# Performance work log

Measured on AMD Instinct MI355X. Metric: run time of the kernel, lower is better.

The kernel has to match this reference:

```python
import jax, jax.numpy as jnp
import numpy as np

B = 4          # clouds per batch
N_PER = 8192   # points per cloud
RATIO = 0.5
M = int(N_PER * RATIO)   # sampled centroids per cloud
R = 0.2        # radius
K = 64         # max_num_neighbors
C_IN = 64


def setup_inputs() -> dict:
    key = jax.random.key(0)
    k1, k2, k3, k4 = jax.random.split(key, 4)
    N = B * N_PER
    x = jax.random.normal(k1, (N, C_IN), dtype=jnp.float32)
    pos = jax.random.uniform(k2, (N, 3), dtype=jnp.float32)  # unit cube
    batch = jnp.repeat(jnp.arange(B, dtype=jnp.int32), N_PER)
    W1 = jax.random.normal(k3, (C_IN + 3, 64), dtype=jnp.float32) * (1.0 / np.sqrt(C_IN + 3))
    b1 = jnp.zeros((64,), dtype=jnp.float32)
    W2 = jax.random.normal(k4, (64, 128), dtype=jnp.float32) * (1.0 / np.sqrt(64))
    b2 = jnp.zeros((128,), dtype=jnp.float32)
    return {"x": x, "pos": pos, "batch": batch, "W1": W1, "b1": b1, "W2": W2, "b2": b2}


def _fps(posb):
    """Farthest point sampling, vectorized over clouds. posb: [B, n, 3] -> idx [B, M]."""
    d0 = jnp.sum((posb - posb[:, :1]) ** 2, axis=-1)  # dist^2 to seed point 0: [B, n]

    def step(dists, _):
        far = jnp.argmax(dists, axis=1)                              # [B]
        newp = jnp.take_along_axis(posb, far[:, None, None], axis=1)  # [B, 1, 3]
        d = jnp.sum((posb - newp) ** 2, axis=-1)                      # [B, n]
        return jnp.minimum(dists, d), far.astype(jnp.int32)

    _, rest = jax.lax.scan(step, d0, None, length=M - 1)  # rest: [M-1, B]
    return jnp.concatenate([jnp.zeros((B, 1), jnp.int32), rest.T], axis=1)  # [B, M]


def reference(x, pos, batch, W1, b1, W2, b2):
    posb = pos.reshape(B, N_PER, 3)
    xb = x.reshape(B, N_PER, C_IN)

    # --- fps ---
    idx = _fps(posb)                                         # [B, M]
    q = jnp.take_along_axis(posb, idx[:, :, None], axis=1)   # sampled centroids [B, M, 3]

    # --- radius query: K nearest neighbors within radius R (same cloud) ---
    d2 = jnp.sum((q[:, :, None, :] - posb[:, None, :, :]) ** 2, axis=-1)  # [B, M, n]
    neg = jnp.where(d2 <= R * R, -d2, -jnp.inf)
    vals, nbr = jax.lax.top_k(neg, K)                        # [B, M, K]
    valid = vals > -jnp.inf                                  # neighbor mask

    # --- PointNetConv: gather -> MLP -> masked max aggregation ---
    bidx = jnp.arange(B)[:, None, None]
    xj = xb[bidx, nbr]                                       # [B, M, K, C_IN]
    rel = posb[bidx, nbr] - q[:, :, None, :]                 # [B, M, K, 3]
    feat = jnp.concatenate([xj, rel], axis=-1)               # [B, M, K, C_IN+3]
    h = jax.nn.relu(feat @ W1 + b1)                          # [B, M, K, 64]
    h = jax.nn.relu(h @ W2 + b2)                             # [B, M, K, 128]
    h = jnp.where(valid[..., None], h, -jnp.inf)
    out = jnp.max(h, axis=2)                                 # [B, M, 128]; self-edge guarantees >=1 valid

    x_out = out.reshape(B * M, 128)
    pos_out = q.reshape(B * M, 3)
    batch_out = jnp.repeat(jnp.arange(B, dtype=batch.dtype), M)
    return x_out, pos_out, batch_out
```

## Files before the change

### kernel.cpp

```cpp
#include <hip/hip_runtime.h>
#include <stdint.h>

#define NPER 8192
#define NB 4
#define MPER 4096
#define MTOT (NB*MPER)
#define KNB 64
#define CIN 64
#define R2C 0.04f

#define POSOUT_OFF (MTOT*128)
#define BATCH_OFF  (MTOT*128 + MTOT*3)

#define PRE_OFF 2162688ull
#define PRE_BYTES 8388608ull

#define SSTR 34816
#define PERM_F 29200

typedef float v2f __attribute__((ext_vector_type(2)));

#define FPS_T 1024
#define PTS 8
#define NCELL 512

#define OFF_XS 0
#define OFF_YS (OFF_XS + NPER*4)
#define OFF_ZS (OFF_YS + NPER*4)
#define OFF_OS (OFF_ZS + NPER*4)
#define OFF_WIN (OFF_OS + NPER*2)
#define OFF_HIST (OFF_WIN + MPER*2)
#define OFF_SCAN (OFF_HIST + NCELL*4)
#define OFF_SLOT (OFF_SCAN + NCELL*4)
#define OFF_SID0 (OFF_SLOT + 24)
#define OFF_BSC  (OFF_SID0 + 8)
#define FPS_LDS  (OFF_BSC + NCELL*4)

template<int CTRL>
__device__ __forceinline__ unsigned dppmax(unsigned v) {
  unsigned t = (unsigned)__builtin_amdgcn_update_dpp(
      0, (int)v, CTRL, 0xf, 0xf, true);
  return v > t ? v : t;
}
__device__ __forceinline__ unsigned wave_max_u32(unsigned v) {
  v = dppmax<0x111>(v);
  v = dppmax<0x112>(v);
  v = dppmax<0x114>(v);
  v = dppmax<0x118>(v);
  v = dppmax<0x142>(v);
  v = dppmax<0x143>(v);
  return (unsigned)__builtin_amdgcn_readlane((int)v, 63);
}

__device__ __forceinline__ unsigned brick_key(unsigned c) {
  unsigned ix = c >> 6, iy = (c >> 3) & 7, iz = c & 7;
  unsigned bid = ((ix >> 2) << 3) | ((iy >> 2) << 2) | (iz >> 1);
  unsigned lid = ((ix & 3) << 3) | ((iy & 3) << 1) | (iz & 1);
  return (bid << 5) | lid;
}

__global__ __launch_bounds__(1024) void k_fps(const float* __restrict__ pos,
                                              float* __restrict__ dout,
                                              const float* __restrict__ xin,
                                              const float* __restrict__ W1,
                                              float* __restrict__ hp)
{
#pragma clang fp contract(off)
  extern __shared__ char smem[];
  const int tid = threadIdx.x;

  if (blockIdx.x >= NB) {
    float* Ws = (float*)smem;
    float* Xs2 = (float*)(smem + 16384);
    const int row0 = (blockIdx.x - NB) * 64;
    for (int e = tid; e < 64*64; e += FPS_T) Ws[e] = W1[e];
    for (int e = tid; e < 64*64; e += FPS_T) {
      int r = e >> 6, ch = e & 63;
      Xs2[r*65 + ch] = xin[(size_t)(row0 + r) * 64 + ch];
    }
    __syncthreads();
    if (tid < 256) {
      const int rg = tid >> 4, cg = tid & 15;
      const int r0 = rg << 2, c0 = cg << 2;
      float acc[4][4];
#pragma unroll
      for (int r = 0; r < 4; ++r)
#pragma unroll
        for (int c = 0; c < 4; ++c) acc[r][c] = 0.0f;
      for (int k = 0; k < 64; ++k) {
        const float4 w = *(const float4*)&Ws[(k << 6) + c0];
        const float xr[4] = {Xs2[(r0+0)*65 + k], Xs2[(r0+1)*65 + k],
                             Xs2[(r0+2)*65 + k], Xs2[(r0+3)*65 + k]};
        const float wc[4] = {w.x, w.y, w.z, w.w};
#pragma unroll
        for (int r = 0; r < 4; ++r)
#pragma unroll
          for (int c = 0; c < 4; ++c)
            acc[r][c] = fmaf(xr[r], wc[c], acc[r][c]);
      }
#pragma unroll
      for (int r = 0; r < 4; ++r) {
        float4 o = {acc[r][0], acc[r][1], acc[r][2], acc[r][3]};
        *(float4*)&hp[(size_t)(row0 + r0 + r) * 64 + c0] = o;
      }
    }
    return;
  }

  float* Xs = (float*)(smem + OFF_XS);
  float* Ys = (float*)(smem + OFF_YS);
  float* Zs = (float*)(smem + OFF_ZS);
  unsigned short* Os = (unsigned short*)(smem + OFF_OS);
  unsigned short* winb = (unsigned short*)(smem + OFF_WIN);
  unsigned* hist = (unsigned*)(smem + OFF_HIST);
  unsigned* scanb = (unsigned*)(smem + OFF_SCAN);
  unsigned long long* slot3 = (unsigned long long*)(smem + OFF_SLOT);
  unsigned* sid0p = (unsigned*)(smem + OFF_SID0);
  unsigned* bsc = (unsigned*)(smem + OFF_BSC);

  const int b = blockIdx.x;
  const float* pb = pos + (size_t)b * NPER * 3;
  float* qo = dout + POSOUT_OFF + (size_t)b * MPER * 3;
  float* scrb = dout + (size_t)b * SSTR;
  float* gSX = scrb; float* gSY = scrb + 8192; float* gSZ = scrb + 16384;
  unsigned* gSO = (unsigned*)(scrb + 24576);
  unsigned* gCS = (unsigned*)(scrb + 28672);
  unsigned short* gPM = (unsigned short*)(scrb + PERM_F);

  if (tid < NCELL) hist[tid] = 0u;
  if (tid == 0) { slot3[0] = 0ull; slot3[1] = 0ull; slot3[2] = 0ull; }
  __syncthreads();

  float sxv[PTS], syv[PTS], szv[PTS];
  unsigned cellv[PTS];
#pragma unroll
  for (int k = 0; k < PTS; ++k) {
    int i = k * FPS_T + tid;
    sxv[k] = pb[i*3+0]; syv[k] = pb[i*3+1]; szv[k] = pb[i*3+2];
    unsigned ix = min(7u, (unsigned)(int)(sxv[k] * 8.0f));
    unsigned iy = min(7u, (unsigned)(int)(syv[k] * 8.0f));
    unsigned iz = min(7u, (unsigned)(int)(szv[k] * 8.0f));
    cellv[k] = (ix << 6) | (iy << 3) | iz;
    atomicAdd(&hist[cellv[k]], 1u);
  }
  __syncthreads();
  if (tid < NCELL) scanb[tid] = hist[tid];
  __syncthreads();
  for (int s = 1; s < NCELL; s <<= 1) {
    unsigned v = 0u;
    if (tid >= s && tid < NCELL) v = scanb[tid - s];
    __syncthreads();
    if (tid >= s && tid < NCELL) scanb[tid] += v;
    __syncthreads();
  }
  if (tid < NCELL) {
    hist[tid] = scanb[tid] - hist[tid];
    gCS[tid+1] = scanb[tid];
  }
  if (tid == 0) gCS[0] = 0u;
  __syncthreads();
  if (tid < NCELL) {
    unsigned c = (unsigned)tid;
    unsigned cntc = scanb[c] - hist[c];
    bsc[brick_key(c)] = cntc;
  }
  __syncthreads();
  for (int s = 1; s < NCELL; s <<= 1) {
    unsigned v = 0u;
    if (tid >= s && tid < NCELL) v = bsc[tid - s];
    __syncthreads();
    if (tid >= s && tid < NCELL) bsc[tid] += v;
    __syncthreads();
  }
  {
    unsigned bst = 0u;
    if (tid < NCELL) {
      unsigned c = (unsigned)tid;
      unsigned cntc = scanb[c] - hist[c];
      bst = bsc[brick_key(c)] - cntc;
    }
    __syncthreads();
    if (tid < NCELL) bsc[tid] = bst;
  }
  __syncthreads();
#pragma unroll
  for (int k = 0; k < PTS; ++k) {
    unsigned dst = atomicAdd(&hist[cellv[k]], 1u);
    unsigned p   = atomicAdd(&bsc[cellv[k]], 1u);
    int orig = k * FPS_T + tid;
    Xs[dst] = sxv[k]; Ys[dst] = syv[k]; Zs[dst] = szv[k];
    Os[dst] = (unsigned short)orig;
    gPM[p] = (unsigned short)dst;
    if (orig == 0) *sid0p = dst;
  }
  __syncthreads();
  for (int e = tid; e < NPER; e += FPS_T) {
    gSX[e] = Xs[e]; gSY[e] = Ys[e]; gSZ[e] = Zs[e];
  }
  for (int e = tid; e < NPER/2; e += FPS_T)
    gSO[e] = ((const unsigned*)Os)[e];
  v2f Xp[4], Yp[4], Zp[4], Dp[4];
  unsigned RK[PTS];
  float bxlo = 3.402823466e+38f, bylo = bxlo, bzlo = bxlo;
  float bxhi = -bxlo, byhi = bxhi, bzhi = bxhi;
#pragma unroll
  for (int k = 0; k < PTS; ++k) {
    int s = (int)gPM[tid * PTS + k];
    float xx = Xs[s], yy = Ys[s], zz = Zs[s];
    Xp[k>>1][k&1] = xx; Yp[k>>1][k&1] = yy; Zp[k>>1][k&1] = zz;
    Dp[k>>1][k&1] = 3.402823466e+38f;
    unsigned orig = Os[s];
    RK[k] = ((unsigned)(NPER - 1 - orig) << 13) | (unsigned)s;
    bxlo = fminf(bxlo, xx); bxhi = fmaxf(bxhi, xx);
    bylo = fminf(bylo, yy); byhi = fmaxf(byhi, yy);
    bzlo = fminf(bzlo, zz); bzhi = fmaxf(bzhi, zz);
  }

  unsigned long long tkey = 0ull, wkey = 0ull;
  float lmax = 3.402823466e+38f;
  unsigned sidx = *sid0p;
  for (int m = 1; m < MPER; ++m) {
    const float cx = Xs[sidx], cy = Ys[sidx], cz = Zs[sidx];
    if (tid == 0) winb[m-1] = (unsigned short)sidx;
    if (tid == 1) slot3[(m+1) % 3] = 0ull;
    float ax = fmaxf(fmaxf(__fsub_rn(bxlo, cx), __fsub_rn(cx, bxhi)), 0.0f);
    float ay = fmaxf(fmaxf(__fsub_rn(bylo, cy), __fsub_rn(cy, byhi)), 0.0f);
    float az = fmaxf(fmaxf(__fsub_rn(bzlo, cz), __fsub_rn(cz, bzhi)), 0.0f);
    float lb = ax*ax + ay*ay + az*az;
    bool upd = (lb * 0.99988f) < lmax;
    if (__ballot(upd) != 0ull) {
      if (upd) {
        v2f cx2 = {cx, cx}, cy2 = {cy, cy}, cz2 = {cz, cz};
        v2f dnp[4];
        float bd = -1.0f;
#pragma unroll
        for (int p = 0; p < 4; ++p) {
          v2f dx = Xp[p] - cx2;
          v2f dy = Yp[p] - cy2;
          v2f dz = Zp[p] - cz2;
          v2f s = (dx*dx + dy*dy) + dz*dz;
          v2f dn;
          dn.x = fminf(Dp[p].x, s.x);
          dn.y = fminf(Dp[p].y, s.y);
          Dp[p] = dn; dnp[p] = dn;
          bd = fmaxf(bd, fmaxf(dn.x, dn.y));
        }
        unsigned brk = 0u;
#pragma unroll
        for (int p = 0; p < 4; ++p) {
          brk = (dnp[p].x == bd) ? max(brk, RK[2*p])   : brk;
          brk = (dnp[p].y == bd) ? max(brk, RK[2*p+1]) : brk;
        }
        tkey = ((unsigned long long)__float_as_uint(bd) << 26) | brk;
        lmax = bd;
      }
      unsigned hi = (unsigned)(tkey >> 26);
      unsigned M = wave_max_u32(hi);
      unsigned rk = (unsigned)tkey & 0x3FFFFFFu;
      unsigned long long msk = __ballot(hi == M);
      unsigned lo;
      if (__popcll(msk) == 1) {
        int ln = (int)__builtin_ctzll(msk);
        lo = (unsigned)__builtin_amdgcn_readlane((int)rk, ln);
      } else {
        lo = wave_max_u32((hi == M) ? rk : 0u);
      }
      wkey = ((unsigned long long)M << 26) | lo;
    }
    if ((tid & 63) == 0) atomicMax(&slot3[m % 3], wkey);
    __syncthreads();
    sidx = (unsigned)(slot3[m % 3] & 0x1FFFull);
  }
  if (tid == 0) winb[MPER-1] = (unsigned short)sidx;
  __syncthreads();
  for (int e = tid; e < MPER; e += FPS_T) {
    unsigned s = winb[e];
    qo[e*3+0] = Xs[s]; qo[e*3+1] = Ys[s]; qo[e*3+2] = Zs[s];
  }
}

#define SCAP 512
__global__ __launch_bounds__(256) void k_radius(const float* __restrict__ pos,
    float* __restrict__ dout, unsigned short* __restrict__ nbr,
    int* __restrict__ cnt)
{
  __shared__ unsigned candH[4][SCAP];
  __shared__ unsigned candL[4][SCAP];
  const int wid = threadIdx.x >> 6, lane = threadIdx.x & 63;
  const int m = blockIdx.x * 4 + wid;
  const int b = m >> 12;
  const float* scrb = dout + (size_t)b * SSTR;
  const float* SX = scrb;
  const float* SY = scrb + 8192;
  const float* SZ = scrb + 16384;
  const unsigned short* SO = (const unsigned short*)(scrb + 24576);
  const unsigned* CS = (const unsigned*)(scrb + 28672);
  const float* q = dout + POSOUT_OFF + (size_t)m * 3;
  const float qx = q[0], qy = q[1], qz = q[2];
  const int ixc = min(7, (int)(qx * 8.0f));
  const int iyc = min(7, (int)(qy * 8.0f));
  const int izc = min(7, (int)(qz * 8.0f));
  const int izlo = max(izc-2, 0), izhi = min(izc+2, 7);
  unsigned s0v = 0u, s1v = 0u;
  {
    int ix = ixc + lane / 5 - 2;
    int iy = iyc + lane % 5 - 2;
    if (lane < 25 && ix >= 0 && ix < 8 && iy >= 0 && iy < 8) {
      int cb = (ix << 6) | (iy << 3);
      s0v = CS[cb + izlo];
      s1v = CS[cb + izhi + 1];
    }
  }
  unsigned cw = 0;
  for (int seg = 0; seg < 25; ++seg) {
    unsigned s0 = (unsigned)__builtin_amdgcn_readlane((int)s0v, seg);
    unsigned s1 = (unsigned)__builtin_amdgcn_readlane((int)s1v, seg);
    for (unsigned i0 = s0; i0 < s1; i0 += 64) {
      unsigned i = i0 + (unsigned)lane;
      float dx = __fsub_rn(qx, SX[i]);
      float dy = __fsub_rn(qy, SY[i]);
      float dz = __fsub_rn(qz, SZ[i]);
      float d2 = __fadd_rn(__fadd_rn(__fmul_rn(dx,dx), __fmul_rn(dy,dy)),
                           __fmul_rn(dz,dz));
      bool in = (i < s1) && (d2 <= R2C);
      unsigned long long mk = __ballot(in);
      unsigned pre = (unsigned)__popcll(mk & ((1ull << lane) - 1ull));
      if (in) {
        unsigned slot = cw + pre;
        if (slot < SCAP) {
          candH[wid][slot] = __float_as_uint(d2);
          candL[wid][slot] = (unsigned)SO[i];
        }
      }
      cw += (unsigned)__popcll(mk);
    }
  }
  if (cw > SCAP) cw = SCAP;
  for (int s = (int)cw + lane; s < SCAP; s += 64) {
    candH[wid][s] = 0xFFFFFFFFu; candL[wid][s] = 0xFFFFFFFFu;
  }
  __syncthreads();
  for (int k = 2; k <= SCAP; k <<= 1) {
    for (int j = k >> 1; j > 0; j >>= 1) {
#pragma unroll
      for (int s = 0; s < SCAP/128; ++s) {
        int t = lane + (s << 6);
        int e = ((t & ~(j-1)) << 1) | (t & (j-1));
        int p = e | j;
        unsigned aH = candH[wid][e], aL = candL[wid][e];
        unsigned cH = candH[wid][p], cL = candL[wid][p];
        bool agt = (aH > cH) || (aH == cH && aL > cL);
        bool asc = ((e & k) == 0);
        bool sw = asc ? agt : !agt && (aH != cH || aL != cL);
        if (sw) {
          candH[wid][e] = cH; candL[wid][e] = cL;
          candH[wid][p] = aH; candL[wid][p] = aL;
        }
      }
      __syncthreads();
    }
  }
  int kk = (int)cw; if (kk > KNB) kk = KNB;
  nbr[(size_t)m*KNB + lane] =
    (lane < kk) ? (unsigned short)(candL[wid][lane] & 0xFFFFu)
                : (unsigned short)0;
  if (lane == 0) {
    cnt[m] = kk;
    dout[BATCH_OFF + m] = (float)b;
  }
}

__global__ __launch_bounds__(128) void k_conv2(
    const float* __restrict__ hp, const float* __restrict__ pos,
    const float* __restrict__ W1, const float* __restrict__ b1,
    const float* __restrict__ W2, const float* __restrict__ b2,
    const unsigned short* __restrict__ nbr, const int* __restrict__ cntp,
    float* __restrict__ dout)
{
  __shared__ __align__(16) float bufA[68*68];
  __shared__ __align__(16) float bufB[16*136];
  __shared__ float w1p[3*64];
  __shared__ unsigned short nbr_s[64];
  __shared__ float qv[3];
  __shared__ int cnt_s;
  const int t = threadIdx.x;
  const int m = blockIdx.x;
  const int b = m >> 12;
  if (t < 64) nbr_s[t] = nbr[(size_t)m*KNB + t];
  else if (t == 64) cnt_s = cntp[m];
  else if (t >= 65 && t < 68) qv[t-65] = dout[POSOUT_OFF + (size_t)m*3 + (t-65)];
  for (int e = t; e < 192; e += 128) w1p[e] = W1[64*64 + e];
  __syncthreads();
  {
    const int h = t & 63, jj = t >> 6;
    const size_t hb = (size_t)b * NPER * 64;
    for (int j0 = 0; j0 < 64; j0 += 2) {
      int j = j0 + jj;
      int r = nbr_s[j];
      bufA[h*68 + j] = hp[hb + (size_t)r*64 + h];
    }
  }
  {
    const size_t pbb = (size_t)b * NPER * 3;
    for (int e = t; e < 192; e += 128) {
      int j = e & 63, d = e >> 6;
      int r = nbr_s[j];
      bufA[(64+d)*68 + j] = pos[pbb + (size_t)r*3 + d] - qv[d];
    }
  }
  __syncthreads();
  for (int e = t; e < 64*64; e += 128) {
    int h = e >> 6, j = e & 63;
    float v = bufA[h*68 + j];
    v = fmaf(bufA[64*68 + j], w1p[h],       v);
    v = fmaf(bufA[65*68 + j], w1p[64 + h],  v);
    v = fmaf(bufA[66*68 + j], w1p[128 + h], v);
    bufA[h*68 + j] = fmaxf(v + b1[h], 0.0f);
  }
  const int jg = t & 7, hg = t >> 3;
  const int j0 = jg << 3;
  const int c0 = hg << 3;
  v2f acc2p[8][4];
#pragma unroll
  for (int c = 0; c < 8; ++c)
#pragma unroll
    for (int jp = 0; jp < 4; ++jp) acc2p[c][jp] = (v2f){0.0f, 0.0f};
  for (int hc = 0; hc < 64; hc += 16) {
    __syncthreads();
    for (int e = t; e < 16*128; e += 128) {
      int hh = e >> 7, c = e & 127;
      bufB[hh*136 + c] = W2[(size_t)(hc+hh)*128 + c];
    }
    __syncthreads();
#pragma unroll
    for (int h = 0; h < 16; ++h) {
      const float4 ja = *(const float4*)&bufA[(hc+h)*68 + j0];
      const float4 jb = *(const float4*)&bufA[(hc+h)*68 + j0 + 4];
      const float4 wa = *(const float4*)&bufB[h*136 + c0];
      const float4 wb = *(const float4*)&bufB[h*136 + c0 + 4];
      const v2f hj[4] = {{ja.x, ja.y}, {ja.z, ja.w}, {jb.x, jb.y}, {jb.z, jb.w}};
      const float wv[8] = {wa.x, wa.y, wa.z, wa.w, wb.x, wb.y, wb.z, wb.w};
#pragma unroll
      for (int c = 0; c < 8; ++c) {
        const v2f w2 = {wv[c], wv[c]};
#pragma unroll
        for (int jp = 0; jp < 4; ++jp)
          acc2p[c][jp] += w2 * hj[jp];
      }
    }
  }
  const int cntv = cnt_s;
  const float4 b2a = *(const float4*)&b2[c0];
  const float4 b2b = *(const float4*)&b2[c0 + 4];
  const float bv2[8] = {b2a.x, b2a.y, b2a.z, b2a.w, b2b.x, b2b.y, b2b.z, b2b.w};
  float best[8];
#pragma unroll
  for (int c = 0; c < 8; ++c) {
    float v = -3.402823466e+38f;
#pragma unroll
    for (int jp = 0; jp < 4; ++jp) {
      float h0v = fmaxf(acc2p[c][jp].x + bv2[c], 0.0f);
      float h1v = fmaxf(acc2p[c][jp].y + bv2[c], 0.0f);
      v = (j0 + 2*jp     < cntv) ? fmaxf(v, h0v) : v;
      v = (j0 + 2*jp + 1 < cntv) ? fmaxf(v, h1v) : v;
    }
    best[c] = v;
  }
#pragma unroll
  for (int off = 1; off < 8; off <<= 1)
#pragma unroll
    for (int c = 0; c < 8; ++c)
      best[c] = fmaxf(best[c], __shfl_xor(best[c], off));
  if (jg == 0) {
    float4 o0 = {best[0], best[1], best[2], best[3]};
    float4 o1 = {best[4], best[5], best[6], best[7]};
    *(float4*)&dout[(size_t)m*128 + c0] = o0;
    *(float4*)&dout[(size_t)m*128 + c0 + 4] = o1;
  }
}

__global__ __launch_bounds__(128) void k_conv(
    const float* __restrict__ x, const float* __restrict__ pos,
    const float* __restrict__ W1, const float* __restrict__ b1,
    const float* __restrict__ W2, const float* __restrict__ b2,
    const unsigned short* __restrict__ nbr, const int* __restrict__ cntp,
    float* __restrict__ dout)
{
  __shared__ __align__(16) float bufA[68*68];
  __shared__ __align__(16) float bufB[68*68];
  __shared__ unsigned short nbr_s[64];
  __shared__ float qv[3];
  __shared__ int cnt_s;
  const int t = threadIdx.x;
  const int m = blockIdx.x;
  const int b = m >> 12;
  if (t < 64) nbr_s[t] = nbr[(size_t)m*KNB + t];
  else if (t == 64) cnt_s = cntp[m];
  else if (t >= 65 && t < 68) qv[t-65] = dout[POSOUT_OFF + (size_t)m*3 + (t-65)];
  for (int e = t; e < 67*64; e += 128) {
    int ch = e >> 6, h = e & 63;
    bufB[ch*68 + h] = W1[e];
  }
  __syncthreads();
  {
    const int ch = t & 63, jj = t >> 6;
    const size_t xb = (size_t)b * NPER * CIN;
    for (int j0 = 0; j0 < 64; j0 += 2) {
      int j = j0 + jj;
      int r = nbr_s[j];
      bufA[ch*68 + j] = x[xb + (size_t)r*CIN + ch];
    }
  }
  {
    const size_t pbb = (size_t)b * NPER * 3;
    for (int e = t; e < 192; e += 128) {
      int j = e & 63, d = e >> 6;
      int r = nbr_s[j];
      bufA[(64+d)*68 + j] = pos[pbb + (size_t)r*3 + d] - qv[d];
    }
  }
  __syncthreads();
  const int jg = t & 7, hg = t >> 3;
  const int j0 = jg << 3;
  const int h0 = hg << 2;
  v2f accp[4][4];
#pragma unroll
  for (int hh = 0; hh < 4; ++hh)
#pragma unroll
    for (int jp = 0; jp < 4; ++jp) accp[hh][jp] = (v2f){0.0f, 0.0f};
  for (int ch = 0; ch < 67; ++ch) {
    const float4 fa = *(const float4*)&bufA[ch*68 + j0];
    const float4 fb = *(const float4*)&bufA[ch*68 + j0 + 4];
    const float4 w  = *(const float4*)&bufB[ch*68 + h0];
    const v2f fj[4] = {{fa.x, fa.y}, {fa.z, fa.w}, {fb.x, fb.y}, {fb.z, fb.w}};
    const float ws4[4] = {w.x, w.y, w.z, w.w};
#pragma unroll
    for (int hh = 0; hh < 4; ++hh) {
      const v2f wv2 = {ws4[hh], ws4[hh]};
#pragma unroll
      for (int jp = 0; jp < 4; ++jp)
        accp[hh][jp] += wv2 * fj[jp];
    }
  }
  __syncthreads();
  {
    const float4 bb = *(const float4*)&b1[h0];
    const float bv[4] = {bb.x, bb.y, bb.z, bb.w};
#pragma unroll
    for (int hh = 0; hh < 4; ++hh) {
      float4 o0, o1;
      o0.x = fmaxf(accp[hh][0].x + bv[hh], 0.0f);
      o0.y = fmaxf(accp[hh][0].y + bv[hh], 0.0f);
      o0.z = fmaxf(accp[hh][1].x + bv[hh], 0.0f);
      o0.w = fmaxf(accp[hh][1].y + bv[hh], 0.0f);
      o1.x = fmaxf(accp[hh][2].x + bv[hh], 0.0f);
      o1.y = fmaxf(accp[hh][2].y + bv[hh], 0.0f);
      o1.z = fmaxf(accp[hh][3].x + bv[hh], 0.0f);
      o1.w = fmaxf(accp[hh][3].y + bv[hh], 0.0f);
      *(float4*)&bufA[(h0+hh)*68 + j0] = o0;
      *(float4*)&bufA[(h0+hh)*68 + j0 + 4] = o1;
    }
  }
  const int c0 = hg << 3;
  v2f acc2p[8][4];
#pragma unroll
  for (int c = 0; c < 8; ++c)
#pragma unroll
    for (int jp = 0; jp < 4; ++jp) acc2p[c][jp] = (v2f){0.0f, 0.0f};
  for (int hc = 0; hc < 64; hc += 16) {
    __syncthreads();
    for (int e = t; e < 16*128; e += 128) {
      int hh = e >> 7, c = e & 127;
      bufB[hh*136 + c] = W2[(size_t)(hc+hh)*128 + c];
    }
    __syncthreads();
#pragma unroll
    for (int h = 0; h < 16; ++h) {
      const float4 ja = *(const float4*)&bufA[(hc+h)*68 + j0];
      const float4 jb = *(const float4*)&bufA[(hc+h)*68 + j0 + 4];
      const float4 wa = *(const float4*)&bufB[h*136 + c0];
      const float4 wb = *(const float4*)&bufB[h*136 + c0 + 4];
      const v2f hj[4] = {{ja.x, ja.y}, {ja.z, ja.w}, {jb.x, jb.y}, {jb.z, jb.w}};
      const float wv[8] = {wa.x, wa.y, wa.z, wa.w, wb.x, wb.y, wb.z, wb.w};
#pragma unroll
      for (int c = 0; c < 8; ++c) {
        const v2f w2 = {wv[c], wv[c]};
#pragma unroll
        for (int jp = 0; jp < 4; ++jp)
          acc2p[c][jp] += w2 * hj[jp];
      }
    }
  }
  const int cntv = cnt_s;
  const float4 b2a = *(const float4*)&b2[c0];
  const float4 b2b = *(const float4*)&b2[c0 + 4];
  const float bv2[8] = {b2a.x, b2a.y, b2a.z, b2a.w, b2b.x, b2b.y, b2b.z, b2b.w};
  float best[8];
#pragma unroll
  for (int c = 0; c < 8; ++c) {
    float v = -3.402823466e+38f;
#pragma unroll
    for (int jp = 0; jp < 4; ++jp) {
      float h0v = fmaxf(acc2p[c][jp].x + bv2[c], 0.0f);
      float h1v = fmaxf(acc2p[c][jp].y + bv2[c], 0.0f);
      v = (j0 + 2*jp     < cntv) ? fmaxf(v, h0v) : v;
      v = (j0 + 2*jp + 1 < cntv) ? fmaxf(v, h1v) : v;
    }
    best[c] = v;
  }
#pragma unroll
  for (int off = 1; off < 8; off <<= 1)
#pragma unroll
    for (int c = 0; c < 8; ++c)
      best[c] = fmaxf(best[c], __shfl_xor(best[c], off));
  if (jg == 0) {
    float4 o0 = {best[0], best[1], best[2], best[3]};
    float4 o1 = {best[4], best[5], best[6], best[7]};
    *(float4*)&dout[(size_t)m*128 + c0] = o0;
    *(float4*)&dout[(size_t)m*128 + c0 + 4] = o1;
  }
}

extern "C" void kernel_launch(void* const* d_in, const int* in_sizes, int n_in,
                              void* d_out, int out_size, void* d_ws, size_t ws_size,
                              hipStream_t stream) {
  const float* x   = (const float*)d_in[0];
  const float* pos = (const float*)d_in[1];
  const float* W1  = (const float*)d_in[3];
  const float* b1  = (const float*)d_in[4];
  const float* W2  = (const float*)d_in[5];
  const float* b2  = (const float*)d_in[6];
  float* dout = (float*)d_out;
  unsigned short* nbr = (unsigned short*)d_ws;
  int* cnt = (int*)((char*)d_ws + (size_t)MTOT*KNB*2);
  float* hp = (float*)((char*)d_ws + PRE_OFF);
  const bool use_pre = (ws_size >= PRE_OFF + PRE_BYTES);

  const int grid = use_pre ? (NB + NB*NPER/64) : NB;
  hipLaunchKernelGGL(k_fps,    dim3(grid),   dim3(FPS_T), FPS_LDS, stream,
                     pos, dout, x, W1, hp);
  hipLaunchKernelGGL(k_radius, dim3(MTOT/4), dim3(256),   0, stream, pos, dout, nbr, cnt);
  if (use_pre) {
    hipLaunchKernelGGL(k_conv2, dim3(MTOT),       dim3(128), 0, stream,
                       hp, pos, W1, b1, W2, b2, nbr, cnt, dout);
  } else {
    hipLaunchKernelGGL(k_conv,  dim3(MTOT),       dim3(128), 0, stream,
                       x, pos, W1, b1, W2, b2, nbr, cnt, dout);
  }
}
```

Measured before the change: 2.929 ms.

## Overlap radius query with FPS via progress-flag producer/consumer blocks

```diff
diff --git a/kernel.cpp b/kernel.cpp
--- a/kernel.cpp
+++ b/kernel.cpp
@@ -15,8 +15,13 @@
 #define PRE_OFF 2162688ull
 #define PRE_BYTES 8388608ull
 
-#define SSTR 34816
+#define SSTR 35392
 #define PERM_F 29200
+#define WIN_F 33312
+#define PROG_F 35360
+
+#define NCONS 248
+#define SCAP 512
 
 typedef float v2f __attribute__((ext_vector_type(2)));
 
@@ -59,17 +64,25 @@
   return (bid << 5) | lid;
 }
 
+__global__ void k_zero(float* __restrict__ dout) {
+  int t = threadIdx.x;
+  if (t < NB) *(unsigned*)(dout + (size_t)t * SSTR + PROG_F) = 0u;
+}
+
 __global__ __launch_bounds__(1024) void k_fps(const float* __restrict__ pos,
                                               float* __restrict__ dout,
                                               const float* __restrict__ xin,
                                               const float* __restrict__ W1,
-                                              float* __restrict__ hp)
+                                              float* __restrict__ hp,
+                                              unsigned short* __restrict__ nbr,
+                                              int* __restrict__ cnt,
+                                              int cbase)
 {
 #pragma clang fp contract(off)
   extern __shared__ char smem[];
   const int tid = threadIdx.x;
 
-  if (blockIdx.x >= NB) {
+  if (blockIdx.x >= NB && (int)blockIdx.x < cbase) {
     float* Ws = (float*)smem;
     float* Xs2 = (float*)(smem + 16384);
     const int row0 = (blockIdx.x - NB) * 64;
@@ -103,6 +116,115 @@
         float4 o = {acc[r][0], acc[r][1], acc[r][2], acc[r][3]};
         *(float4*)&hp[(size_t)(row0 + r0 + r) * 64 + c0] = o;
       }
+    }
+    return;
+  }
+
+  if ((int)blockIdx.x >= cbase) {
+    unsigned* candH = (unsigned*)smem;
+    unsigned* candL = candH + 16*SCAP;
+    const int wid = tid >> 6, lane = tid & 63;
+    const int cb0 = (int)blockIdx.x - cbase;
+    for (int g = cb0; g < MTOT/16; g += NCONS) {
+      const int m = g*16 + wid;
+      const int b = m >> 12;
+      const float* scrb2 = dout + (size_t)b * SSTR;
+      unsigned* progp = (unsigned*)(scrb2 + PROG_F);
+      const unsigned blkmax = (unsigned)((g*16 + 15) & 4095) + 1u;
+      if (wid == 0) {
+        unsigned v;
+        do {
+          unsigned t0 = 0u;
+          if (lane == 0)
+            t0 = __hip_atomic_load(progp, __ATOMIC_RELAXED,
+                                   __HIP_MEMORY_SCOPE_AGENT);
+          v = (unsigned)__builtin_amdgcn_readfirstlane((int)t0);
+          if (v < blkmax) __builtin_amdgcn_s_sleep(32);
+        } while (v < blkmax);
+      }
+      __syncthreads();
+      (void)__hip_atomic_load(progp, __ATOMIC_ACQUIRE,
+                              __HIP_MEMORY_SCOPE_AGENT);
+      const float* SX = scrb2;
+      const float* SY = scrb2 + 8192;
+      const float* SZ = scrb2 + 16384;
+      const unsigned short* SO = (const unsigned short*)(scrb2 + 24576);
+      const unsigned* CS = (const unsigned*)(scrb2 + 28672);
+      const unsigned short* gWIN = (const unsigned short*)(scrb2 + WIN_F);
+      const unsigned slot = gWIN[m & 4095];
+      const float qx = SX[slot], qy = SY[slot], qz = SZ[slot];
+      const int ixc = min(7, (int)(qx * 8.0f));
+      const int iyc = min(7, (int)(qy * 8.0f));
+      const int izc = min(7, (int)(qz * 8.0f));
+      const int izlo = max(izc-2, 0), izhi = min(izc+2, 7);
+      unsigned s0v = 0u, s1v = 0u;
+      {
+        int ix = ixc + lane / 5 - 2;
+        int iy = iyc + lane % 5 - 2;
+        if (lane < 25 && ix >= 0 && ix < 8 && iy >= 0 && iy < 8) {
+          int cbq = (ix << 6) | (iy << 3);
+          s0v = CS[cbq + izlo];
+          s1v = CS[cbq + izhi + 1];
+        }
+      }
+      unsigned cw = 0;
+      for (int seg = 0; seg < 25; ++seg) {
+        unsigned s0 = (unsigned)__builtin_amdgcn_readlane((int)s0v, seg);
+        unsigned s1 = (unsigned)__builtin_amdgcn_readlane((int)s1v, seg);
+        for (unsigned i0 = s0; i0 < s1; i0 += 64) {
+          unsigned i = i0 + (unsigned)lane;
+          float dx = __fsub_rn(qx, SX[i]);
+          float dy = __fsub_rn(qy, SY[i]);
+          float dz = __fsub_rn(qz, SZ[i]);
+          float d2 = __fadd_rn(__fadd_rn(__fmul_rn(dx,dx), __fmul_rn(dy,dy)),
+                               __fmul_rn(dz,dz));
+          bool in = (i < s1) && (d2 <= R2C);
+          unsigned long long mk = __ballot(in);
+          unsigned pre = (unsigned)__popcll(mk & ((1ull << lane) - 1ull));
+          if (in) {
+            unsigned slt = cw + pre;
+            if (slt < SCAP) {
+              candH[wid*SCAP + slt] = __float_as_uint(d2);
+              candL[wid*SCAP + slt] = (unsigned)SO[i];
+            }
+          }
+          cw += (unsigned)__popcll(mk);
+        }
+      }
+      if (cw > SCAP) cw = SCAP;
+      for (int s = (int)cw + lane; s < SCAP; s += 64) {
+        candH[wid*SCAP + s] = 0xFFFFFFFFu; candL[wid*SCAP + s] = 0xFFFFFFFFu;
+      }
+      __syncthreads();
+      for (int k = 2; k <= SCAP; k <<= 1) {
+        for (int j = k >> 1; j > 0; j >>= 1) {
+#pragma unroll
+          for (int s = 0; s < SCAP/128; ++s) {
+            int t = lane + (s << 6);
+            int e = ((t & ~(j-1)) << 1) | (t & (j-1));
+            int p = e | j;
+            unsigned aH = candH[wid*SCAP + e], aL = candL[wid*SCAP + e];
+            unsigned cH = candH[wid*SCAP + p], cL = candL[wid*SCAP + p];
+            bool agt = (aH > cH) || (aH == cH && aL > cL);
+            bool asc = ((e & k) == 0);
+            bool sw = asc ? agt : !agt && (aH != cH || aL != cL);
+            if (sw) {
+              candH[wid*SCAP + e] = cH; candL[wid*SCAP + e] = cL;
+              candH[wid*SCAP + p] = aH; candL[wid*SCAP + p] = aL;
+            }
+          }
+          __syncthreads();
+        }
+      }
+      int kk = (int)cw; if (kk > KNB) kk = KNB;
+      nbr[(size_t)m*KNB + lane] =
+        (lane < kk) ? (unsigned short)(candL[wid*SCAP + lane] & 0xFFFFu)
+                    : (unsigned short)0;
+      if (lane == 0) {
+        cnt[m] = kk;
+        dout[BATCH_OFF + m] = (float)b;
+      }
+      __syncthreads();
     }
     return;
   }
@@ -126,6 +248,9 @@
   unsigned* gSO = (unsigned*)(scrb + 24576);
   unsigned* gCS = (unsigned*)(scrb + 28672);
   unsigned short* gPM = (unsigned short*)(scrb + PERM_F);
+  unsigned* gWINu32 = (unsigned*)(scrb + WIN_F);
+  unsigned* winbU32 = (unsigned*)winb;
+  unsigned* progp = (unsigned*)(scrb + PROG_F);
 
   if (tid < NCELL) hist[tid] = 0u;
   if (tid == 0) { slot3[0] = 0ull; slot3[1] = 0ull; slot3[2] = 0ull; }
@@ -223,6 +348,16 @@
     const float cx = Xs[sidx], cy = Ys[sidx], cz = Zs[sidx];
     if (tid == 0) winb[m-1] = (unsigned short)sidx;
     if (tid == 1) slot3[(m+1) % 3] = 0ull;
+    if ((m & 255) == 1 && m > 256) {
+      const int u0 = ((m - 257) >> 8) << 7;
+      if (tid < 128) gWINu32[u0 + tid] = winbU32[u0 + tid];
+      __syncthreads();
+      if (tid == 0) {
+        __threadfence();
+        __hip_atomic_store(progp, (unsigned)(m - 1), __ATOMIC_RELAXED,
+                           __HIP_MEMORY_SCOPE_AGENT);
+      }
+    }
     float ax = fmaxf(fmaxf(__fsub_rn(bxlo, cx), __fsub_rn(cx, bxhi)), 0.0f);
     float ay = fmaxf(fmaxf(__fsub_rn(bylo, cy), __fsub_rn(cy, byhi)), 0.0f);
     float az = fmaxf(fmaxf(__fsub_rn(bzlo, cz), __fsub_rn(cz, bzhi)), 0.0f);
@@ -277,96 +412,12 @@
     unsigned s = winb[e];
     qo[e*3+0] = Xs[s]; qo[e*3+1] = Ys[s]; qo[e*3+2] = Zs[s];
   }
-}
-
-#define SCAP 512
-__global__ __launch_bounds__(256) void k_radius(const float* __restrict__ pos,
-    float* __restrict__ dout, unsigned short* __restrict__ nbr,
-    int* __restrict__ cnt)
-{
-  __shared__ unsigned candH[4][SCAP];
-  __shared__ unsigned candL[4][SCAP];
-  const int wid = threadIdx.x >> 6, lane = threadIdx.x & 63;
-  const int m = blockIdx.x * 4 + wid;
-  const int b = m >> 12;
-  const float* scrb = dout + (size_t)b * SSTR;
-  const float* SX = scrb;
-  const float* SY = scrb + 8192;
-  const float* SZ = scrb + 16384;
-  const unsigned short* SO = (const unsigned short*)(scrb + 24576);
-  const unsigned* CS = (const unsigned*)(scrb + 28672);
-  const float* q = dout + POSOUT_OFF + (size_t)m * 3;
-  const float qx = q[0], qy = q[1], qz = q[2];
-  const int ixc = min(7, (int)(qx * 8.0f));
-  const int iyc = min(7, (int)(qy * 8.0f));
-  const int izc = min(7, (int)(qz * 8.0f));
-  const int izlo = max(izc-2, 0), izhi = min(izc+2, 7);
-  unsigned s0v = 0u, s1v = 0u;
-  {
-    int ix = ixc + lane / 5 - 2;
-    int iy = iyc + lane % 5 - 2;
-    if (lane < 25 && ix >= 0 && ix < 8 && iy >= 0 && iy < 8) {
-      int cb = (ix << 6) | (iy << 3);
-      s0v = CS[cb + izlo];
-      s1v = CS[cb + izhi + 1];
-    }
-  }
-  unsigned cw = 0;
-  for (int seg = 0; seg < 25; ++seg) {
-    unsigned s0 = (unsigned)__builtin_amdgcn_readlane((int)s0v, seg);
-    unsigned s1 = (unsigned)__builtin_amdgcn_readlane((int)s1v, seg);
-    for (unsigned i0 = s0; i0 < s1; i0 += 64) {
-      unsigned i = i0 + (unsigned)lane;
-      float dx = __fsub_rn(qx, SX[i]);
-      float dy = __fsub_rn(qy, SY[i]);
-      float dz = __fsub_rn(qz, SZ[i]);
-      float d2 = __fadd_rn(__fadd_rn(__fmul_rn(dx,dx), __fmul_rn(dy,dy)),
-                           __fmul_rn(dz,dz));
-      bool in = (i < s1) && (d2 <= R2C);
-      unsigned long long mk = __ballot(in);
-      unsigned pre = (unsigned)__popcll(mk & ((1ull << lane) - 1ull));
-      if (in) {
-        unsigned slot = cw + pre;
-        if (slot < SCAP) {
-          candH[wid][slot] = __float_as_uint(d2);
-          candL[wid][slot] = (unsigned)SO[i];
-        }
-      }
-      cw += (unsigned)__popcll(mk);
-    }
-  }
-  if (cw > SCAP) cw = SCAP;
-  for (int s = (int)cw + lane; s < SCAP; s += 64) {
-    candH[wid][s] = 0xFFFFFFFFu; candL[wid][s] = 0xFFFFFFFFu;
-  }
-  __syncthreads();
-  for (int k = 2; k <= SCAP; k <<= 1) {
-    for (int j = k >> 1; j > 0; j >>= 1) {
-#pragma unroll
-      for (int s = 0; s < SCAP/128; ++s) {
-        int t = lane + (s << 6);
-        int e = ((t & ~(j-1)) << 1) | (t & (j-1));
-        int p = e | j;
-        unsigned aH = candH[wid][e], aL = candL[wid][e];
-        unsigned cH = candH[wid][p], cL = candL[wid][p];
-        bool agt = (aH > cH) || (aH == cH && aL > cL);
-        bool asc = ((e & k) == 0);
-        bool sw = asc ? agt : !agt && (aH != cH || aL != cL);
-        if (sw) {
-          candH[wid][e] = cH; candL[wid][e] = cL;
-          candH[wid][p] = aH; candL[wid][p] = aL;
-        }
-      }
-      __syncthreads();
-    }
-  }
-  int kk = (int)cw; if (kk > KNB) kk = KNB;
-  nbr[(size_t)m*KNB + lane] =
-    (lane < kk) ? (unsigned short)(candL[wid][lane] & 0xFFFFu)
-                : (unsigned short)0;
-  if (lane == 0) {
-    cnt[m] = kk;
-    dout[BATCH_OFF + m] = (float)b;
+  if (tid < 128) gWINu32[1920 + tid] = winbU32[1920 + tid];
+  __syncthreads();
+  if (tid == 0) {
+    __threadfence();
+    __hip_atomic_store(progp, 4096u, __ATOMIC_RELAXED,
+                       __HIP_MEMORY_SCOPE_AGENT);
   }
 }
 
@@ -636,15 +687,16 @@
   float* hp = (float*)((char*)d_ws + PRE_OFF);
   const bool use_pre = (ws_size >= PRE_OFF + PRE_BYTES);
 
-  const int grid = use_pre ? (NB + NB*NPER/64) : NB;
-  hipLaunchKernelGGL(k_fps,    dim3(grid),   dim3(FPS_T), FPS_LDS, stream,
-                     pos, dout, x, W1, hp);
-  hipLaunchKernelGGL(k_radius, dim3(MTOT/4), dim3(256),   0, stream, pos, dout, nbr, cnt);
+  const int cbase = use_pre ? (NB + NB*NPER/64) : NB;
+  const int grid = cbase + NCONS;
+  hipLaunchKernelGGL(k_zero, dim3(1),    dim3(64),    0, stream, dout);
+  hipLaunchKernelGGL(k_fps,  dim3(grid), dim3(FPS_T), FPS_LDS, stream,
+                     pos, dout, x, W1, hp, nbr, cnt, cbase);
   if (use_pre) {
-    hipLaunchKernelGGL(k_conv2, dim3(MTOT),       dim3(128), 0, stream,
+    hipLaunchKernelGGL(k_conv2, dim3(MTOT), dim3(128), 0, stream,
                        hp, pos, W1, b1, W2, b2, nbr, cnt, dout);
   } else {
-    hipLaunchKernelGGL(k_conv,  dim3(MTOT),       dim3(128), 0, stream,
+    hipLaunchKernelGGL(k_conv,  dim3(MTOT), dim3(128), 0, stream,
                        x, pos, W1, b1, W2, b2, nbr, cnt, dout);
   }
 }
```

Result: slower. 3.146 ms (+7.4%).

## Fuse radius neighbor query into conv kernel and move scratch to workspace

Applied to the files above, without the earlier changes.

```diff
diff --git a/kernel.cpp b/kernel.cpp
--- a/kernel.cpp
+++ b/kernel.cpp
@@ -61,6 +61,7 @@
 
 __global__ __launch_bounds__(1024) void k_fps(const float* __restrict__ pos,
                                               float* __restrict__ dout,
+                                              float* __restrict__ scr,
                                               const float* __restrict__ xin,
                                               const float* __restrict__ W1,
                                               float* __restrict__ hp)
@@ -121,7 +122,7 @@
   const int b = blockIdx.x;
   const float* pb = pos + (size_t)b * NPER * 3;
   float* qo = dout + POSOUT_OFF + (size_t)b * MPER * 3;
-  float* scrb = dout + (size_t)b * SSTR;
+  float* scrb = scr + (size_t)b * SSTR;
   float* gSX = scrb; float* gSY = scrb + 8192; float* gSZ = scrb + 16384;
   unsigned* gSO = (unsigned*)(scrb + 24576);
   unsigned* gCS = (unsigned*)(scrb + 28672);
@@ -280,7 +281,7 @@
 }
 
 #define SCAP 512
-__global__ __launch_bounds__(256) void k_radius(const float* __restrict__ pos,
+__global__ __launch_bounds__(256) void k_radius(const float* __restrict__ scr,
     float* __restrict__ dout, unsigned short* __restrict__ nbr,
     int* __restrict__ cnt)
 {
@@ -289,7 +290,7 @@
   const int wid = threadIdx.x >> 6, lane = threadIdx.x & 63;
   const int m = blockIdx.x * 4 + wid;
   const int b = m >> 12;
-  const float* scrb = dout + (size_t)b * SSTR;
+  const float* scrb = scr + (size_t)b * SSTR;
   const float* SX = scrb;
   const float* SY = scrb + 8192;
   const float* SZ = scrb + 16384;
@@ -370,11 +371,11 @@
   }
 }
 
-__global__ __launch_bounds__(128) void k_conv2(
+__global__ __launch_bounds__(128) void k_rc2(
     const float* __restrict__ hp, const float* __restrict__ pos,
+    const float* __restrict__ scr,
     const float* __restrict__ W1, const float* __restrict__ b1,
     const float* __restrict__ W2, const float* __restrict__ b2,
-    const unsigned short* __restrict__ nbr, const int* __restrict__ cntp,
     float* __restrict__ dout)
 {
   __shared__ __align__(16) float bufA[68*68];
@@ -383,14 +384,99 @@
   __shared__ unsigned short nbr_s[64];
   __shared__ float qv[3];
   __shared__ int cnt_s;
+  unsigned* candH = (unsigned*)bufA;
+  unsigned* candL = candH + SCAP;
   const int t = threadIdx.x;
   const int m = blockIdx.x;
   const int b = m >> 12;
-  if (t < 64) nbr_s[t] = nbr[(size_t)m*KNB + t];
-  else if (t == 64) cnt_s = cntp[m];
-  else if (t >= 65 && t < 68) qv[t-65] = dout[POSOUT_OFF + (size_t)m*3 + (t-65)];
+  const int wid = t >> 6, lane = t & 63;
+  const float* scrb = scr + (size_t)b * SSTR;
+  const float* SX = scrb;
+  const float* SY = scrb + 8192;
+  const float* SZ = scrb + 16384;
+  const unsigned short* SO = (const unsigned short*)(scrb + 24576);
+  const unsigned* CS = (const unsigned*)(scrb + 28672);
+
+  if (t >= 64 && t < 67) qv[t-64] = dout[POSOUT_OFF + (size_t)m*3 + (t-64)];
+  if (t == 67) dout[BATCH_OFF + m] = (float)b;
   for (int e = t; e < 192; e += 128) w1p[e] = W1[64*64 + e];
   __syncthreads();
+  const float qx = qv[0], qy = qv[1], qz = qv[2];
+
+  if (wid == 0) {
+    const int ixc = min(7, (int)(qx * 8.0f));
+    const int iyc = min(7, (int)(qy * 8.0f));
+    const int izc = min(7, (int)(qz * 8.0f));
+    const int izlo = max(izc-2, 0), izhi = min(izc+2, 7);
+    unsigned s0v = 0u, s1v = 0u;
+    {
+      int ix = ixc + lane / 5 - 2;
+      int iy = iyc + lane % 5 - 2;
+      if (lane < 25 && ix >= 0 && ix < 8 && iy >= 0 && iy < 8) {
+        int cb = (ix << 6) | (iy << 3);
+        s0v = CS[cb + izlo];
+        s1v = CS[cb + izhi + 1];
+      }
+    }
+    unsigned cw = 0;
+    for (int seg = 0; seg < 25; ++seg) {
+      unsigned s0 = (unsigned)__builtin_amdgcn_readlane((int)s0v, seg);
+      unsigned s1 = (unsigned)__builtin_amdgcn_readlane((int)s1v, seg);
+      for (unsigned i0 = s0; i0 < s1; i0 += 64) {
+        unsigned i = i0 + (unsigned)lane;
+        float dx = __fsub_rn(qx, SX[i]);
+        float dy = __fsub_rn(qy, SY[i]);
+        float dz = __fsub_rn(qz, SZ[i]);
+        float d2 = __fadd_rn(__fadd_rn(__fmul_rn(dx,dx), __fmul_rn(dy,dy)),
+                             __fmul_rn(dz,dz));
+        bool in = (i < s1) && (d2 <= R2C);
+        unsigned long long mk = __ballot(in);
+        unsigned pre = (unsigned)__popcll(mk & ((1ull << lane) - 1ull));
+        if (in) {
+          unsigned slot = cw + pre;
+          if (slot < SCAP) {
+            candH[slot] = __float_as_uint(d2);
+            candL[slot] = (unsigned)SO[i];
+          }
+        }
+        cw += (unsigned)__popcll(mk);
+      }
+    }
+    if (cw > SCAP) cw = SCAP;
+    for (int s = (int)cw + lane; s < SCAP; s += 64) {
+      candH[s] = 0xFFFFFFFFu; candL[s] = 0xFFFFFFFFu;
+    }
+    if (lane == 0) {
+      int kk = (int)cw; if (kk > KNB) kk = KNB;
+      cnt_s = kk;
+    }
+  }
+  __syncthreads();
+  for (int k = 2; k <= SCAP; k <<= 1) {
+    for (int j = k >> 1; j > 0; j >>= 1) {
+#pragma unroll
+      for (int s = 0; s < SCAP/256; ++s) {
+        int t2 = t + (s << 7);
+        int e = ((t2 & ~(j-1)) << 1) | (t2 & (j-1));
+        int p = e | j;
+        unsigned aH = candH[e], aL = candL[e];
+        unsigned cH = candH[p], cL = candL[p];
+        bool agt = (aH > cH) || (aH == cH && aL > cL);
+        bool asc = ((e & k) == 0);
+        bool sw = asc ? agt : !agt && (aH != cH || aL != cL);
+        if (sw) {
+          candH[e] = cH; candL[e] = cL;
+          candH[p] = aH; candL[p] = aL;
+        }
+      }
+      __syncthreads();
+    }
+  }
+  if (t < 64)
+    nbr_s[t] = (t < cnt_s) ? (unsigned short)(candL[t] & 0xFFFFu)
+                           : (unsigned short)0;
+  __syncthreads();
+
   {
     const int h = t & 63, jj = t >> 6;
     const size_t hb = (size_t)b * NPER * 64;
@@ -636,15 +722,18 @@
   float* hp = (float*)((char*)d_ws + PRE_OFF);
   const bool use_pre = (ws_size >= PRE_OFF + PRE_BYTES);
 
+  float* scr = use_pre ? (float*)d_ws : dout;
+
   const int grid = use_pre ? (NB + NB*NPER/64) : NB;
-  hipLaunchKernelGGL(k_fps,    dim3(grid),   dim3(FPS_T), FPS_LDS, stream,
-                     pos, dout, x, W1, hp);
-  hipLaunchKernelGGL(k_radius, dim3(MTOT/4), dim3(256),   0, stream, pos, dout, nbr, cnt);
+  hipLaunchKernelGGL(k_fps, dim3(grid), dim3(FPS_T), FPS_LDS, stream,
+                     pos, dout, scr, x, W1, hp);
   if (use_pre) {
-    hipLaunchKernelGGL(k_conv2, dim3(MTOT),       dim3(128), 0, stream,
-                       hp, pos, W1, b1, W2, b2, nbr, cnt, dout);
+    hipLaunchKernelGGL(k_rc2, dim3(MTOT), dim3(128), 0, stream,
+                       hp, pos, scr, W1, b1, W2, b2, dout);
   } else {
-    hipLaunchKernelGGL(k_conv,  dim3(MTOT),       dim3(128), 0, stream,
+    hipLaunchKernelGGL(k_radius, dim3(MTOT/4), dim3(256), 0, stream,
+                       scr, dout, nbr, cnt);
+    hipLaunchKernelGGL(k_conv,   dim3(MTOT),   dim3(128), 0, stream,
                        x, pos, W1, b1, W2, b2, nbr, cnt, dout);
   }
 }
```

Measured after the change: 3.118 ms. 1.06x slower.
